# Kernel optimization log

Measured on AMD Instinct MI355X. Metric: run time of the kernel, lower is better.

Reference implementation:

```python
import jax, jax.numpy as jnp
import numpy as np

N, D, H, C, F = 100000, 128, 4, 32, 512  # nodes, hidden, heads, per-head out, ffn dim
E = 600000
NEG_SLOPE = 0.2
LN_EPS = 1e-5


def setup_inputs() -> dict:
    key = jax.random.key(0)
    ks = iter(jax.random.split(key, 32))
    nrm = lambda shape, s=0.05: jax.random.normal(next(ks), shape, dtype=jnp.float32) * s
    inp = {
        "x": jax.random.normal(next(ks), (N, D), dtype=jnp.float32),
        "edge_index": jax.random.randint(next(ks), (2, E), 0, N, dtype=jnp.int64),
    }
    for p in ("c1", "c2"):
        inp[p + "_wl"] = nrm((D, H * C))
        inp[p + "_bl"] = jnp.zeros((H * C,), jnp.float32)
        inp[p + "_wr"] = nrm((D, H * C))
        inp[p + "_br"] = jnp.zeros((H * C,), jnp.float32)
        inp[p + "_att"] = nrm((H, C))
        inp[p + "_bias"] = jnp.zeros((H * C,), jnp.float32)
    for p in ("f1", "f2"):
        inp[p + "_w1"] = nrm((D, F))
        inp[p + "_b1"] = jnp.zeros((F,), jnp.float32)
        inp[p + "_w2"] = nrm((F, D))
        inp[p + "_b2"] = jnp.zeros((D,), jnp.float32)
    for p in ("ln1", "ln2"):
        inp[p + "_g"] = jnp.ones((D,), jnp.float32)
        inp[p + "_b"] = jnp.zeros((D,), jnp.float32)
    return inp


def gatv2(x, src, dst, wl, bl, wr, br, att, bias):
    # per-node linear transforms (source uses lin_l, target uses lin_r)
    xl = (x @ wl + bl).reshape(N, H, C)
    xr = (x @ wr + br).reshape(N, H, C)
    e = jax.nn.leaky_relu(xl[src] + xr[dst], NEG_SLOPE)       # [E,H,C]
    alpha = jnp.einsum("ehc,hc->eh", e, att)                  # [E,H]
    # numerically-stable segment softmax over edges grouped by target node
    amax = jax.ops.segment_max(alpha, dst, num_segments=N)    # [N,H]
    ex = jnp.exp(alpha - amax[dst])
    denom = jax.ops.segment_sum(ex, dst, num_segments=N)      # [N,H]
    a = ex / (denom[dst] + 1e-16)
    msg = xl[src] * a[:, :, None]                             # [E,H,C]
    out = jax.ops.segment_sum(msg, dst, num_segments=N)       # [N,H,C]
    return out.reshape(N, H * C) + bias


def layer_norm(x, g, b):
    mu = jnp.mean(x, axis=-1, keepdims=True)
    var = jnp.var(x, axis=-1, keepdims=True)
    return (x - mu) * jax.lax.rsqrt(var + LN_EPS) * g + b


def ffn(x, w1, b1, w2, b2):
    return jax.nn.relu(x @ w1 + b1) @ w2 + b2


def reference(x, edge_index,
              c1_wl, c1_bl, c1_wr, c1_br, c1_att, c1_bias,
              c2_wl, c2_bl, c2_wr, c2_br, c2_att, c2_bias,
              f1_w1, f1_b1, f1_w2, f1_b2,
              f2_w1, f2_b1, f2_w2, f2_b2,
              ln1_g, ln1_b, ln2_g, ln2_b):
    src, dst = edge_index[0], edge_index[1]
    h = gatv2(x, src, dst, c1_wl, c1_bl, c1_wr, c1_br, c1_att, c1_bias)
    h = layer_norm(h + ffn(h, f1_w1, f1_b1, f1_w2, f1_b2), ln1_g, ln1_b)
    h = gatv2(h, src, dst, c2_wl, c2_bl, c2_wr, c2_br, c2_att, c2_bias)
    h = layer_norm(h + ffn(h, f2_w1, f2_b1, f2_w2, f2_b2), ln2_g, ln2_b)
    return h
```

## Files before the change

### kernel.cpp

```cpp
#include <hip/hip_runtime.h>

#define NN 100000
#define DD 128
#define EE 600000
#define LNEPS 1e-5f

__device__ __forceinline__ float lrelu(float v) { return v > 0.f ? v : 0.2f * v; }

__global__ __launch_bounds__(256) void lin_kernel(
    const float* __restrict__ x,
    const float* __restrict__ wl, const float* __restrict__ bl,
    const float* __restrict__ wr, const float* __restrict__ br,
    float* __restrict__ xl, float* __restrict__ xr)
{
    __shared__ __align__(16) float xs[64][128];
    const int tid  = threadIdx.x;
    const int row0 = blockIdx.x * 64;
#pragma unroll
    for (int i = 0; i < 32; ++i) {
        int idx = tid + i * 256;
        int r = idx >> 7, c = idx & 127;
        int row = row0 + r;
        xs[r][c] = (row < NN) ? x[(size_t)row * DD + c] : 0.f;
    }
    __syncthreads();
    const int cg = tid & 63;
    const int rg = tid >> 6;
    float acc[16][4];
    {
        float b0 = bl[cg], b1 = bl[cg + 64], b2 = br[cg], b3 = br[cg + 64];
#pragma unroll
        for (int r = 0; r < 16; ++r) { acc[r][0] = b0; acc[r][1] = b1; acc[r][2] = b2; acc[r][3] = b3; }
    }
    for (int k = 0; k < 128; k += 4) {
        float wa[4], wb[4], wc[4], wd[4];
#pragma unroll
        for (int i = 0; i < 4; ++i) {
            wa[i] = wl[(k + i) * DD + cg];
            wb[i] = wl[(k + i) * DD + cg + 64];
            wc[i] = wr[(k + i) * DD + cg];
            wd[i] = wr[(k + i) * DD + cg + 64];
        }
#pragma unroll
        for (int r = 0; r < 16; ++r) {
            float4 xv = *(const float4*)&xs[rg * 16 + r][k];
            acc[r][0] = fmaf(xv.x, wa[0], fmaf(xv.y, wa[1], fmaf(xv.z, wa[2], fmaf(xv.w, wa[3], acc[r][0]))));
            acc[r][1] = fmaf(xv.x, wb[0], fmaf(xv.y, wb[1], fmaf(xv.z, wb[2], fmaf(xv.w, wb[3], acc[r][1]))));
            acc[r][2] = fmaf(xv.x, wc[0], fmaf(xv.y, wc[1], fmaf(xv.z, wc[2], fmaf(xv.w, wc[3], acc[r][2]))));
            acc[r][3] = fmaf(xv.x, wd[0], fmaf(xv.y, wd[1], fmaf(xv.z, wd[2], fmaf(xv.w, wd[3], acc[r][3]))));
        }
    }
#pragma unroll
    for (int r = 0; r < 16; ++r) {
        int row = row0 + rg * 16 + r;
        if (row < NN) {
            xl[(size_t)row * DD + cg]      = acc[r][0];
            xl[(size_t)row * DD + cg + 64] = acc[r][1];
            xr[(size_t)row * DD + cg]      = acc[r][2];
            xr[(size_t)row * DD + cg + 64] = acc[r][3];
        }
    }
}

__global__ __launch_bounds__(256) void deg_hist_kernel(const int* __restrict__ ei, int* __restrict__ deg)
{
    int e = blockIdx.x * 256 + threadIdx.x;
    if (e < EE) atomicAdd(&deg[ei[EE + e]], 1);
}

__global__ __launch_bounds__(1024) void scan1_kernel(const int* __restrict__ deg,
                                                     int* __restrict__ rowstart,
                                                     int* __restrict__ partials)
{
    int gid = blockIdx.x * 1024 + threadIdx.x;
    int v = (gid < NN) ? deg[gid] : 0;
    int lane = threadIdx.x & 63, wid = threadIdx.x >> 6;
    int s = v;
#pragma unroll
    for (int o = 1; o < 64; o <<= 1) { int t = __shfl_up(s, o); if (lane >= o) s += t; }
    __shared__ int wsum[16];
    if (lane == 63) wsum[wid] = s;
    __syncthreads();
    if (wid == 0 && lane < 16) {
        int w = wsum[lane];
        int ws = w;
#pragma unroll
        for (int o = 1; o < 16; o <<= 1) { int t = __shfl_up(ws, o); if (lane >= o) ws += t; }
        wsum[lane] = ws - w;
    }
    __syncthreads();
    int incl = s + wsum[wid];
    if (gid < NN) rowstart[gid] = incl - v;
    if (threadIdx.x == 1023) partials[blockIdx.x] = incl;
}

__global__ __launch_bounds__(128) void scan2_kernel(int* __restrict__ partials, int nb)
{
    int t = threadIdx.x;
    int v = (t < nb) ? partials[t] : 0;
    int lane = t & 63, wid = t >> 6;
    int s = v;
#pragma unroll
    for (int o = 1; o < 64; o <<= 1) { int tt = __shfl_up(s, o); if (lane >= o) s += tt; }
    __shared__ int wsum[2];
    if (lane == 63) wsum[wid] = s;
    __syncthreads();
    int add = (wid == 1) ? wsum[0] : 0;
    if (t < nb) partials[t] = s + add - v;
}

__global__ __launch_bounds__(1024) void scan3_kernel(int* __restrict__ rowstart, const int* __restrict__ partials)
{
    int gid = blockIdx.x * 1024 + threadIdx.x;
    if (gid < NN) rowstart[gid] += partials[blockIdx.x];
}

__global__ __launch_bounds__(256) void fill_kernel(const int* __restrict__ ei,
                                                   int* __restrict__ cursor,
                                                   int* __restrict__ esrc)
{
    int e = blockIdx.x * 256 + threadIdx.x;
    if (e >= EE) return;
    int dst = ei[EE + e];
    int pos = atomicAdd(&cursor[dst], 1);
    esrc[pos] = ei[e];
}

__global__ __launch_bounds__(256) void gather_kernel(
    const float* __restrict__ xl, const float* __restrict__ xr,
    const int* __restrict__ esrc,
    const int* __restrict__ rowstart, const int* __restrict__ rowend,
    const float* __restrict__ att,
    float* __restrict__ hacc)
{
    int n = blockIdx.x * 4 + (threadIdx.x >> 6);
    if (n >= NN) return;
    int lane = threadIdx.x & 63;
    float2 xrv = *(const float2*)&xr[(size_t)n * DD + lane * 2];
    float2 av  = *(const float2*)&att[lane * 2];
    int s0 = rowstart[n], s1 = rowend[n];
    float accx = 0.f, accy = 0.f, denom = 0.f;
    for (int j = s0; j < s1; ++j) {
        int src = esrc[j];
        float2 xlv = *(const float2*)&xl[(size_t)src * DD + lane * 2];
        float p = lrelu(xlv.x + xrv.x) * av.x + lrelu(xlv.y + xrv.y) * av.y;
#pragma unroll
        for (int m = 1; m < 16; m <<= 1) p += __shfl_xor(p, m);
        float exv = __expf(p);
        denom += exv;
        accx = fmaf(exv, xlv.x, accx);
        accy = fmaf(exv, xlv.y, accy);
    }
    float inv = 1.f / (denom + 1e-16f);
    float2 o; o.x = accx * inv; o.y = accy * inv;
    *(float2*)&hacc[(size_t)n * DD + lane * 2] = o;
}

__global__ __launch_bounds__(256) void ffn_ln_kernel(
    const float* __restrict__ hacc, const float* __restrict__ cbias,
    const float* __restrict__ w1, const float* __restrict__ b1,
    const float* __restrict__ w2, const float* __restrict__ b2,
    const float* __restrict__ g, const float* __restrict__ bb,
    float* __restrict__ out)
{
    __shared__ __align__(16) float hrow[16][128];
    __shared__ __align__(16) float T[16][512];
    __shared__ __align__(16) float ybuf[16][128];
    const int tid  = threadIdx.x;
    const int row0 = blockIdx.x * 16;
#pragma unroll
    for (int i = 0; i < 8; ++i) {
        int idx = tid + i * 256;
        int r = idx >> 7, c = idx & 127;
        hrow[r][c] = hacc[(size_t)(row0 + r) * DD + c] + cbias[c];
    }
    __syncthreads();
    {
        const int f = tid;
        float acc[16][2];
        float ba = b1[f], bcol = b1[f + 256];
#pragma unroll
        for (int r = 0; r < 16; ++r) { acc[r][0] = ba; acc[r][1] = bcol; }
        for (int k = 0; k < 128; k += 4) {
            float wa[4], wb[4];
#pragma unroll
            for (int i = 0; i < 4; ++i) { wa[i] = w1[(k + i) * 512 + f]; wb[i] = w1[(k + i) * 512 + f + 256]; }
#pragma unroll
            for (int r = 0; r < 16; ++r) {
                float4 xv = *(const float4*)&hrow[r][k];
                acc[r][0] = fmaf(xv.x, wa[0], fmaf(xv.y, wa[1], fmaf(xv.z, wa[2], fmaf(xv.w, wa[3], acc[r][0]))));
                acc[r][1] = fmaf(xv.x, wb[0], fmaf(xv.y, wb[1], fmaf(xv.z, wb[2], fmaf(xv.w, wb[3], acc[r][1]))));
            }
        }
#pragma unroll
        for (int r = 0; r < 16; ++r) {
            T[r][f]       = fmaxf(acc[r][0], 0.f);
            T[r][f + 256] = fmaxf(acc[r][1], 0.f);
        }
    }
    __syncthreads();
    {
        const int d  = tid & 127;
        const int kh = tid >> 7;
        float acc[16];
#pragma unroll
        for (int r = 0; r < 16; ++r) acc[r] = 0.f;
        const int k0 = kh * 256;
        for (int k = k0; k < k0 + 256; k += 4) {
            float wv[4];
#pragma unroll
            for (int i = 0; i < 4; ++i) wv[i] = w2[(k + i) * DD + d];
#pragma unroll
            for (int r = 0; r < 16; ++r) {
                float4 tv = *(const float4*)&T[r][k];
                acc[r] = fmaf(tv.x, wv[0], fmaf(tv.y, wv[1], fmaf(tv.z, wv[2], fmaf(tv.w, wv[3], acc[r]))));
            }
        }
        if (kh == 1) {
#pragma unroll
            for (int r = 0; r < 16; ++r) ybuf[r][d] = acc[r];
        }
        __syncthreads();
        if (kh == 0) {
            float bv = b2[d];
#pragma unroll
            for (int r = 0; r < 16; ++r)
                ybuf[r][d] = acc[r] + ybuf[r][d] + bv + hrow[r][d];
        }
    }
    __syncthreads();
    {
        const int wv = tid >> 6, lane = tid & 63;
        for (int r = wv; r < 16; r += 4) {
            float2 yv = *(const float2*)&ybuf[r][lane * 2];
            float s  = yv.x + yv.y;
            float s2 = yv.x * yv.x + yv.y * yv.y;
#pragma unroll
            for (int m = 1; m < 64; m <<= 1) { s += __shfl_xor(s, m); s2 += __shfl_xor(s2, m); }
            float mu  = s * (1.f / 128.f);
            float var = s2 * (1.f / 128.f) - mu * mu;
            float inv = rsqrtf(var + LNEPS);
            float2 gv = *(const float2*)&g[lane * 2];
            float2 bv = *(const float2*)&bb[lane * 2];
            float2 o;
            o.x = (yv.x - mu) * inv * gv.x + bv.x;
            o.y = (yv.y - mu) * inv * gv.y + bv.y;
            *(float2*)&out[(size_t)(row0 + r) * DD + lane * 2] = o;
        }
    }
}

extern "C" void kernel_launch(void* const* d_in, const int* in_sizes, int n_in,
                              void* d_out, int out_size, void* d_ws, size_t ws_size,
                              hipStream_t stream)
{
    const float* x       = (const float*)d_in[0];
    const int*   ei      = (const int*)d_in[1];
    const float* c1_wl   = (const float*)d_in[2];
    const float* c1_bl   = (const float*)d_in[3];
    const float* c1_wr   = (const float*)d_in[4];
    const float* c1_br   = (const float*)d_in[5];
    const float* c1_att  = (const float*)d_in[6];
    const float* c1_bias = (const float*)d_in[7];
    const float* c2_wl   = (const float*)d_in[8];
    const float* c2_bl   = (const float*)d_in[9];
    const float* c2_wr   = (const float*)d_in[10];
    const float* c2_br   = (const float*)d_in[11];
    const float* c2_att  = (const float*)d_in[12];
    const float* c2_bias = (const float*)d_in[13];
    const float* f1_w1   = (const float*)d_in[14];
    const float* f1_b1   = (const float*)d_in[15];
    const float* f1_w2   = (const float*)d_in[16];
    const float* f1_b2   = (const float*)d_in[17];
    const float* f2_w1   = (const float*)d_in[18];
    const float* f2_b1   = (const float*)d_in[19];
    const float* f2_w2   = (const float*)d_in[20];
    const float* f2_b2   = (const float*)d_in[21];
    const float* ln1_g   = (const float*)d_in[22];
    const float* ln1_b   = (const float*)d_in[23];
    const float* ln2_g   = (const float*)d_in[24];
    const float* ln2_b   = (const float*)d_in[25];

    float* out = (float*)d_out;
    float* ws  = (float*)d_ws;
    float* xl    = ws;
    float* xr    = xl   + (size_t)NN * DD;
    float* hacc  = xr   + (size_t)NN * DD;
    int* deg      = (int*)(hacc + (size_t)NN * DD);
    int* rowstart = deg + NN;
    int* cursor   = rowstart + NN;
    int* partials = cursor + NN;
    int* esrc     = partials + 128;

    const dim3 blk(256);
    const int linGrid    = (NN + 63) / 64;
    const int edgeGrid   = (EE + 255) / 256;
    const int gatherGrid = (NN + 3) / 4;
    const int ffnGrid    = NN / 16;
    const int scanBlocks = (NN + 1023) / 1024;

    hipMemsetAsync(deg, 0, (size_t)NN * sizeof(int), stream);
    deg_hist_kernel<<<edgeGrid, blk, 0, stream>>>(ei, deg);
    scan1_kernel<<<scanBlocks, 1024, 0, stream>>>(deg, rowstart, partials);
    scan2_kernel<<<1, 128, 0, stream>>>(partials, scanBlocks);
    scan3_kernel<<<scanBlocks, 1024, 0, stream>>>(rowstart, partials);
    hipMemcpyAsync(cursor, rowstart, (size_t)NN * sizeof(int), hipMemcpyDeviceToDevice, stream);
    fill_kernel<<<edgeGrid, blk, 0, stream>>>(ei, cursor, esrc);

    lin_kernel<<<linGrid, blk, 0, stream>>>(x, c1_wl, c1_bl, c1_wr, c1_br, xl, xr);
    gather_kernel<<<gatherGrid, blk, 0, stream>>>(xl, xr, esrc, rowstart, cursor, c1_att, hacc);
    ffn_ln_kernel<<<ffnGrid, blk, 0, stream>>>(hacc, c1_bias, f1_w1, f1_b1, f1_w2, f1_b2,
                                               ln1_g, ln1_b, out);
    lin_kernel<<<linGrid, blk, 0, stream>>>(out, c2_wl, c2_bl, c2_wr, c2_br, xl, xr);
    gather_kernel<<<gatherGrid, blk, 0, stream>>>(xl, xr, esrc, rowstart, cursor, c2_att, hacc);
    ffn_ln_kernel<<<ffnGrid, blk, 0, stream>>>(hacc, c2_bias, f2_w1, f2_b1, f2_w2, f2_b2,
                                               ln2_g, ln2_b, out);
}
```

Baseline: 1.336 ms.

## Retile FFN GEMMs with 2D register tiles and drop split-K combine

Reworks the fused FFN+LayerNorm kernel so each thread computes a small rows-by-columns register tile in both matmuls instead of row strips. The second matmul no longer splits K across two thread halves, which removes the shared-memory partial-sum combine, and the output buffer reuses the intermediate T array to shrink shared memory. The goal is better weight reuse in GEMM1 and higher occupancy. The trade-off is that GEMM2 now reuses each weight load across only two rows, raising global/L1 load pressure.

Result: slower. 1.446 ms (+8.2%).

```diff
diff --git a/kernel.cpp b/kernel.cpp
--- a/kernel.cpp
+++ b/kernel.cpp
@@ -82,11 +82,11 @@
     if (lane == 63) wsum[wid] = s;
     __syncthreads();
     if (wid == 0 && lane < 16) {
-        int w = wsum[lane];
-        int ws = w;
+        int wv = wsum[lane];
+        int ws = wv;
 #pragma unroll
         for (int o = 1; o < 16; o <<= 1) { int t = __shfl_up(ws, o); if (lane >= o) ws += t; }
-        wsum[lane] = ws - w;
+        wsum[lane] = ws - wv;
     }
     __syncthreads();
     int incl = s + wsum[wid];
@@ -131,7 +131,7 @@
     const int* __restrict__ esrc,
     const int* __restrict__ rowstart, const int* __restrict__ rowend,
     const float* __restrict__ att,
-    float* __restrict__ hacc)
+    float* __restrict__ hout)
 {
     int n = blockIdx.x * 4 + (threadIdx.x >> 6);
     if (n >= NN) return;
@@ -153,86 +153,99 @@
     }
     float inv = 1.f / (denom + 1e-16f);
     float2 o; o.x = accx * inv; o.y = accy * inv;
-    *(float2*)&hacc[(size_t)n * DD + lane * 2] = o;
-}
-
-__global__ __launch_bounds__(256) void ffn_ln_kernel(
-    const float* __restrict__ hacc, const float* __restrict__ cbias,
+    *(float2*)&hout[(size_t)n * DD + lane * 2] = o;
+}
+
+__global__ __launch_bounds__(256) void ffn_ln_f32v3_kernel(
+    const float* __restrict__ hin, const float* __restrict__ cbias,
     const float* __restrict__ w1, const float* __restrict__ b1,
     const float* __restrict__ w2, const float* __restrict__ b2,
     const float* __restrict__ g, const float* __restrict__ bb,
     float* __restrict__ out)
 {
     __shared__ __align__(16) float hrow[16][128];
-    __shared__ __align__(16) float T[16][512];
-    __shared__ __align__(16) float ybuf[16][128];
+    __shared__ __align__(16) float T[16 * 512];
     const int tid  = threadIdx.x;
     const int row0 = blockIdx.x * 16;
 #pragma unroll
     for (int i = 0; i < 8; ++i) {
         int idx = tid + i * 256;
         int r = idx >> 7, c = idx & 127;
-        hrow[r][c] = hacc[(size_t)(row0 + r) * DD + c] + cbias[c];
+        hrow[r][c] = hin[(size_t)(row0 + r) * DD + c] + cbias[c];
     }
     __syncthreads();
     {
-        const int f = tid;
-        float acc[16][2];
-        float ba = b1[f], bcol = b1[f + 256];
-#pragma unroll
-        for (int r = 0; r < 16; ++r) { acc[r][0] = ba; acc[r][1] = bcol; }
+        const int rg = tid >> 7, c4 = tid & 127;
+        float bv[4];
+#pragma unroll
+        for (int j = 0; j < 4; ++j) bv[j] = b1[c4 + 128 * j];
+        float acc[8][4];
+#pragma unroll
+        for (int r = 0; r < 8; ++r)
+#pragma unroll
+            for (int j = 0; j < 4; ++j) acc[r][j] = bv[j];
         for (int k = 0; k < 128; k += 4) {
-            float wa[4], wb[4];
-#pragma unroll
-            for (int i = 0; i < 4; ++i) { wa[i] = w1[(k + i) * 512 + f]; wb[i] = w1[(k + i) * 512 + f + 256]; }
-#pragma unroll
-            for (int r = 0; r < 16; ++r) {
-                float4 xv = *(const float4*)&hrow[r][k];
-                acc[r][0] = fmaf(xv.x, wa[0], fmaf(xv.y, wa[1], fmaf(xv.z, wa[2], fmaf(xv.w, wa[3], acc[r][0]))));
-                acc[r][1] = fmaf(xv.x, wb[0], fmaf(xv.y, wb[1], fmaf(xv.z, wb[2], fmaf(xv.w, wb[3], acc[r][1]))));
+            float wv[4][4];
+#pragma unroll
+            for (int i = 0; i < 4; ++i)
+#pragma unroll
+                for (int j = 0; j < 4; ++j)
+                    wv[i][j] = w1[(size_t)(k + i) * 512 + c4 + 128 * j];
+#pragma unroll
+            for (int r = 0; r < 8; ++r) {
+                float4 h = *(const float4*)&hrow[rg * 8 + r][k];
+#pragma unroll
+                for (int j = 0; j < 4; ++j)
+                    acc[r][j] = fmaf(h.x, wv[0][j], fmaf(h.y, wv[1][j],
+                                fmaf(h.z, wv[2][j], fmaf(h.w, wv[3][j], acc[r][j]))));
             }
         }
 #pragma unroll
-        for (int r = 0; r < 16; ++r) {
-            T[r][f]       = fmaxf(acc[r][0], 0.f);
-            T[r][f + 256] = fmaxf(acc[r][1], 0.f);
-        }
+        for (int r = 0; r < 8; ++r)
+#pragma unroll
+            for (int j = 0; j < 4; ++j)
+                T[(rg * 8 + r) * 512 + c4 + 128 * j] = fmaxf(acc[r][j], 0.f);
     }
     __syncthreads();
     {
-        const int d  = tid & 127;
-        const int kh = tid >> 7;
-        float acc[16];
-#pragma unroll
-        for (int r = 0; r < 16; ++r) acc[r] = 0.f;
-        const int k0 = kh * 256;
-        for (int k = k0; k < k0 + 256; k += 4) {
-            float wv[4];
-#pragma unroll
-            for (int i = 0; i < 4; ++i) wv[i] = w2[(k + i) * DD + d];
-#pragma unroll
-            for (int r = 0; r < 16; ++r) {
-                float4 tv = *(const float4*)&T[r][k];
-                acc[r] = fmaf(tv.x, wv[0], fmaf(tv.y, wv[1], fmaf(tv.z, wv[2], fmaf(tv.w, wv[3], acc[r]))));
+        const int rg = tid >> 5, c = tid & 31;
+        float acc[2][4];
+#pragma unroll
+        for (int r = 0; r < 2; ++r)
+#pragma unroll
+            for (int j = 0; j < 4; ++j) acc[r][j] = 0.f;
+        for (int k = 0; k < 512; k += 4) {
+            float wv[4][4];
+#pragma unroll
+            for (int i = 0; i < 4; ++i)
+#pragma unroll
+                for (int j = 0; j < 4; ++j)
+                    wv[i][j] = w2[(size_t)(k + i) * 128 + c + 32 * j];
+#pragma unroll
+            for (int r = 0; r < 2; ++r) {
+                float4 t = *(const float4*)&T[(rg * 2 + r) * 512 + k];
+#pragma unroll
+                for (int j = 0; j < 4; ++j)
+                    acc[r][j] = fmaf(t.x, wv[0][j], fmaf(t.y, wv[1][j],
+                                fmaf(t.z, wv[2][j], fmaf(t.w, wv[3][j], acc[r][j]))));
             }
         }
-        if (kh == 1) {
-#pragma unroll
-            for (int r = 0; r < 16; ++r) ybuf[r][d] = acc[r];
-        }
         __syncthreads();
-        if (kh == 0) {
-            float bv = b2[d];
-#pragma unroll
-            for (int r = 0; r < 16; ++r)
-                ybuf[r][d] = acc[r] + ybuf[r][d] + bv + hrow[r][d];
-        }
+        float* ybuf = T;
+#pragma unroll
+        for (int r = 0; r < 2; ++r)
+#pragma unroll
+            for (int j = 0; j < 4; ++j) {
+                int row = rg * 2 + r, col = c + 32 * j;
+                ybuf[row * 132 + col] = acc[r][j] + b2[col] + hrow[row][col];
+            }
     }
     __syncthreads();
     {
+        float* ybuf = T;
         const int wv = tid >> 6, lane = tid & 63;
         for (int r = wv; r < 16; r += 4) {
-            float2 yv = *(const float2*)&ybuf[r][lane * 2];
+            float2 yv = *(const float2*)&ybuf[r * 132 + lane * 2];
             float s  = yv.x + yv.y;
             float s2 = yv.x * yv.x + yv.y * yv.y;
 #pragma unroll
@@ -309,10 +322,10 @@
 
     lin_kernel<<<linGrid, blk, 0, stream>>>(x, c1_wl, c1_bl, c1_wr, c1_br, xl, xr);
     gather_kernel<<<gatherGrid, blk, 0, stream>>>(xl, xr, esrc, rowstart, cursor, c1_att, hacc);
-    ffn_ln_kernel<<<ffnGrid, blk, 0, stream>>>(hacc, c1_bias, f1_w1, f1_b1, f1_w2, f1_b2,
-                                               ln1_g, ln1_b, out);
+    ffn_ln_f32v3_kernel<<<ffnGrid, blk, 0, stream>>>(hacc, c1_bias, f1_w1, f1_b1, f1_w2, f1_b2,
+                                                     ln1_g, ln1_b, out);
     lin_kernel<<<linGrid, blk, 0, stream>>>(out, c2_wl, c2_bl, c2_wr, c2_br, xl, xr);
     gather_kernel<<<gatherGrid, blk, 0, stream>>>(xl, xr, esrc, rowstart, cursor, c2_att, hacc);
-    ffn_ln_kernel<<<ffnGrid, blk, 0, stream>>>(hacc, c2_bias, f2_w1, f2_b1, f2_w2, f2_b2,
-                                               ln2_g, ln2_b, out);
-}
+    ffn_ln_f32v3_kernel<<<ffnGrid, blk, 0, stream>>>(hacc, c2_bias, f2_w1, f2_b1, f2_w2, f2_b2,
+                                                     ln2_g, ln2_b, out);
+}
```
